# Optimization experiments

Hardware: AMD Instinct MI355X
Metric: run time of the kernel (lower is better)

The kernel has to match this reference:

```python
import jax, jax.numpy as jnp
import numpy as np

ALPHA = 0.01  # leaky relu slope

def setup_inputs() -> dict:
    key = jax.random.key(0)
    ks = jax.random.split(key, 6)
    B, N1, N2, D_IN, D_OUT = 8, 2048, 2048, 256, 256
    return {
        "input_tensor1": jax.random.normal(ks[0], (B, N1, D_IN), jnp.float32),
        "attention_mask1": jnp.zeros((B, 1, N1), jnp.float32),
        "input_tensor2": jax.random.normal(ks[1], (B, N2, D_IN), jnp.float32),
        "attention_mask2": jnp.zeros((B, 1, N2), jnp.float32),
        "W1": jax.random.normal(ks[2], (D_IN, D_OUT), jnp.float32) * 0.05,
        "a1": jax.random.normal(ks[3], (2 * D_OUT, 1), jnp.float32) * 0.05,
        "W2": jax.random.normal(ks[4], (D_IN, D_OUT), jnp.float32) * 0.05,
        "a2": jax.random.normal(ks[5], (2 * D_OUT, 1), jnp.float32) * 0.05,
    }

def _cross_attn(Wh_q, Wh_k, a, mask):
    d = Wh_q.shape[-1]
    # additive GAT-style scores: [B, Nq, 1] + [B, 1, Nk] -> [B, Nq, Nk]
    s_q = Wh_q @ a[:d, :]            # [B, Nq, 1]
    s_k = Wh_k @ a[d:, :]            # [B, Nk, 1]
    e = s_q + jnp.swapaxes(s_k, -1, -2)
    e = jax.nn.leaky_relu(e, negative_slope=ALPHA)
    probs = jax.nn.softmax(e + mask, axis=-1)
    ctx = probs @ Wh_k               # [B, Nq, d]
    return ctx, probs

def reference(input_tensor1, attention_mask1, input_tensor2, attention_mask2, W1, a1, W2, a2):
    # dropout in eval mode (identity) for a deterministic reference
    Wh11 = input_tensor1 @ W1
    Wh12 = input_tensor2 @ W1
    ctx1, probs1 = _cross_attn(Wh11, Wh12, a1, attention_mask2)
    Wh22 = input_tensor2 @ W2
    Wh21 = input_tensor1 @ W2
    ctx2, probs2 = _cross_attn(Wh22, Wh21, a2, attention_mask1)
    return ctx1, ctx2, probs1, probs2
```

## Files before the change

### kernel.cpp

```cpp
#include <hip/hip_runtime.h>
#include <hip/hip_bf16.h>
#include <stdint.h>

#define ALPHA 0.01f

typedef __attribute__((ext_vector_type(8))) short short8;
typedef __attribute__((ext_vector_type(4))) float f32x4;
typedef __attribute__((ext_vector_type(4))) float float4_;
typedef __attribute__((ext_vector_type(4))) unsigned short ushort4_;
typedef unsigned int u32;

static __device__ __forceinline__ unsigned short f2bf(float f) {
    union { float f; u32 u; } v; v.f = f;
    u32 r = v.u + 0x7FFF + ((v.u >> 16) & 1);
    return (unsigned short)(r >> 16);
}

static __device__ __forceinline__ void lds_load16(const void* g, void* l) {
    __builtin_amdgcn_global_load_lds((const __attribute__((address_space(1))) u32*)g,
                                     (__attribute__((address_space(3))) u32*)l, 16, 0, 0);
}

__global__ __launch_bounds__(256) void k_prep_w(const float* __restrict__ W1, const float* __restrict__ W2,
                                                unsigned short* __restrict__ W1T, unsigned short* __restrict__ W2T) {
    int bb = blockIdx.x;
    const float* W = (bb & 256) ? W2 : W1;
    unsigned short* WT = (bb & 256) ? W2T : W1T;
    int n = bb & 255, k = threadIdx.x;
    WT[n * 256 + k] = f2bf(W[k * 256 + n]);
}

__global__ __launch_bounds__(256) void k_prep_u(const float* __restrict__ W1, const float* __restrict__ a1,
                                                const float* __restrict__ W2, const float* __restrict__ a2,
                                                float* __restrict__ u) {
    int v = blockIdx.x;
    const float* W = (v < 2) ? W1 : W2;
    const float* a = ((v < 2) ? a1 : a2) + (v & 1) * 256;
    int d = threadIdx.x;
    float acc = 0.f;
    for (int n = 0; n < 256; n++) acc += W[d * 256 + n] * a[n];
    u[v * 256 + d] = acc;
}

__global__ __launch_bounds__(256) void k_cast_s(const float* __restrict__ in1, const float* __restrict__ in2,
                                                const float* __restrict__ u,
                                                unsigned short* __restrict__ in1b, unsigned short* __restrict__ in2b,
                                                float* __restrict__ s) {
    int gid = blockIdx.x * 4 + (threadIdx.x >> 6);
    int tensor = gid >> 14;
    int row = gid & 16383;
    int lane = threadIdx.x & 63;
    const float* in = tensor ? in2 : in1;
    unsigned short* outb = tensor ? in2b : in1b;
    const float* uA = u + (tensor ? 256 : 0);
    const float* uB = u + (tensor ? 512 : 768);
    float* sA = s + (tensor ? 1 : 0) * 16384;
    float* sB = s + (tensor ? 2 : 3) * 16384;

    float4_ v = *(const float4_*)(in + row * 256 + lane * 4);
    float4_ ua = *(const float4_*)(uA + lane * 4);
    float4_ ub = *(const float4_*)(uB + lane * 4);
    ushort4_ ob;
    ob.x = f2bf(v.x); ob.y = f2bf(v.y); ob.z = f2bf(v.z); ob.w = f2bf(v.w);
    *(ushort4_*)(outb + row * 256 + lane * 4) = ob;
    float accA = v.x * ua.x + v.y * ua.y + v.z * ua.z + v.w * ua.w;
    float accB = v.x * ub.x + v.y * ub.y + v.z * ub.z + v.w * ub.w;
    for (int off = 32; off; off >>= 1) {
        accA += __shfl_xor(accA, off, 64);
        accB += __shfl_xor(accB, off, 64);
    }
    if (lane == 0) { sA[row] = accA; sB[row] = accB; }
}

__global__ __launch_bounds__(256) void k_gemm_whT(const unsigned short* __restrict__ W1T,
                                                  const unsigned short* __restrict__ W2T,
                                                  const unsigned short* __restrict__ in1b,
                                                  const unsigned short* __restrict__ in2b,
                                                  unsigned short* __restrict__ whT1,
                                                  unsigned short* __restrict__ whT2) {
    __shared__ unsigned short sA[128 * 32];
    __shared__ unsigned short sB[128 * 32];
    int c = blockIdx.x >> 8;
    int bid = blockIdx.x & 255;
    int mt = bid & 1, ntile = bid >> 1;
    const unsigned short* A = c ? W2T : W1T;
    const unsigned short* Bm = c ? in1b : in2b;
    unsigned short* outp = c ? whT2 : whT1;
    int t = threadIdx.x;
    int w = t >> 6, lane = t & 63, l15 = lane & 15, lq = lane >> 4;
    int wm = (w & 1) * 64, wn = (w >> 1) * 64;
    f32x4 acc[4][4] = {};
    const unsigned short* gA = A + (mt * 128 + (t >> 2)) * 256 + (t & 3) * 8;
    const unsigned short* gB = Bm + (ntile * 128 + (t >> 2)) * 256 + (t & 3) * 8;

    for (int kk = 0; kk < 256; kk += 32) {
        lds_load16(gA + kk, &sA[t * 8]);
        lds_load16(gA + kk + 64 * 256, &sA[t * 8 + 2048]);
        lds_load16(gB + kk, &sB[t * 8]);
        lds_load16(gB + kk + 64 * 256, &sB[t * 8 + 2048]);
        __syncthreads();
        short8 af[4], bfr[4];
#pragma unroll
        for (int m2 = 0; m2 < 4; m2++) af[m2] = *(const short8*)&sA[(wm + m2 * 16 + l15) * 32 + lq * 8];
#pragma unroll
        for (int n2 = 0; n2 < 4; n2++) bfr[n2] = *(const short8*)&sB[(wn + n2 * 16 + l15) * 32 + lq * 8];
#pragma unroll
        for (int m2 = 0; m2 < 4; m2++)
#pragma unroll
            for (int n2 = 0; n2 < 4; n2++)
                acc[m2][n2] = __builtin_amdgcn_mfma_f32_16x16x32_bf16(af[m2], bfr[n2], acc[m2][n2], 0, 0, 0);
        __syncthreads();
    }
#pragma unroll
    for (int m2 = 0; m2 < 4; m2++) {
#pragma unroll
        for (int n2 = 0; n2 < 4; n2++) {
            int i_glob = ntile * 128 + wn + n2 * 16 + l15;
            int bb = i_glob >> 11, ii = i_glob & 2047;
#pragma unroll
            for (int r = 0; r < 4; r++) {
                int d = mt * 128 + wm + m2 * 16 + lq * 4 + r;
                outp[bb * (256 * 2048) + d * 2048 + ii] = f2bf(acc[m2][n2][r]);
            }
        }
    }
}

__global__ __launch_bounds__(512) void k_attn(const float* __restrict__ s,
                                              const unsigned short* __restrict__ whT1,
                                              const unsigned short* __restrict__ whT2,
                                              const float* __restrict__ mask1, const float* __restrict__ mask2,
                                              float* __restrict__ out) {
    __shared__ unsigned short sP[128 * 40];
    __shared__ unsigned short sV[256 * 32];
    __shared__ float lsk[2048];
    __shared__ float lmk[2048];
    __shared__ float lsq[128], lm[128], lil[128];

    int lb = (blockIdx.x & 7) * 32 + (blockIdx.x >> 3);
    int a = lb >> 7, b = (lb >> 4) & 7, mt = lb & 15;
    int t = threadIdx.x;
    const float* skp = s + (a ? 3 : 1) * 16384 + b * 2048;
    const float* sqp = s + (a ? 2 : 0) * 16384 + b * 2048 + mt * 128;
    const float* mp = (a ? mask1 : mask2) + b * 2048;
    const unsigned short* V = (a ? whT2 : whT1) + b * (256 * 2048);
    float* pout = out + 8388608 + a * 33554432 + (b * 2048 + mt * 128) * 2048;
    float* cout = out + a * 4194304 + (b * 2048 + mt * 128) * 256;

    for (int j = t; j < 2048; j += 512) { lsk[j] = skp[j]; lmk[j] = mp[j]; }
    if (t < 128) lsq[t] = sqp[t];
    __syncthreads();

    int w = t >> 6, lane = t & 63, l15 = lane & 15, lq = lane >> 4;

    for (int rr = 0; rr < 16; rr++) {
        int row = w * 16 + rr;
        float sq = lsq[row];
        float mx = -3.4e38f;
        for (int j = lane; j < 2048; j += 64) {
            float x = sq + lsk[j];
            x = fmaxf(x, x * ALPHA) + lmk[j];
            mx = fmaxf(mx, x);
        }
        for (int off = 32; off; off >>= 1) mx = fmaxf(mx, __shfl_xor(mx, off, 64));
        float sum = 0.f;
        for (int j = lane; j < 2048; j += 64) {
            float x = sq + lsk[j];
            x = fmaxf(x, x * ALPHA) + lmk[j];
            sum += __expf(x - mx);
        }
        for (int off = 32; off; off >>= 1) sum += __shfl_xor(sum, off, 64);
        if (lane == 0) { lm[row] = mx; lil[row] = 1.0f / sum; }
    }
    __syncthreads();

    int wm = (w & 1) * 64, wn = (w >> 1) * 64;
    f32x4 acc[4][4] = {};
    int pi = t >> 2;
    int pj = (t & 3) * 8;
    const unsigned short* gV = V + (t >> 2) * 2048 + (t & 3) * 8;

    for (int j0 = 0; j0 < 2048; j0 += 32) {
        lds_load16(gV + j0, &sV[t * 8]);
        lds_load16(gV + j0 + 128 * 2048, &sV[t * 8 + 4096]);
        __builtin_amdgcn_sched_barrier(0);

        float sqv = lsq[pi], mv = lm[pi], ilv = lil[pi];
        float pv[8];
#pragma unroll
        for (int q = 0; q < 8; q++) {
            float x = sqv + lsk[j0 + pj + q];
            x = fmaxf(x, x * ALPHA) + lmk[j0 + pj + q];
            pv[q] = __expf(x - mv) * ilv;
        }
        {
            float4_* gp = (float4_*)(pout + pi * 2048 + j0 + pj);
            float4_ v0, v1;
            v0.x = pv[0]; v0.y = pv[1]; v0.z = pv[2]; v0.w = pv[3];
            v1.x = pv[4]; v1.y = pv[5]; v1.z = pv[6]; v1.w = pv[7];
            __builtin_nontemporal_store(v0, gp);
            __builtin_nontemporal_store(v1, gp + 1);
        }
        union { short8 v; unsigned short u[8]; } pk;
#pragma unroll
        for (int q = 0; q < 8; q++) pk.u[q] = f2bf(pv[q]);
        *(short8*)&sP[pi * 40 + pj] = pk.v;

        asm volatile("s_waitcnt vmcnt(2) lgkmcnt(0)" ::: "memory");
        __builtin_amdgcn_s_barrier();

        short8 af[4], bfr[4];
#pragma unroll
        for (int m2 = 0; m2 < 4; m2++) af[m2] = *(const short8*)&sP[(wm + m2 * 16 + l15) * 40 + lq * 8];
#pragma unroll
        for (int n2 = 0; n2 < 4; n2++) bfr[n2] = *(const short8*)&sV[(wn + n2 * 16 + l15) * 32 + lq * 8];
#pragma unroll
        for (int m2 = 0; m2 < 4; m2++)
#pragma unroll
            for (int n2 = 0; n2 < 4; n2++)
                acc[m2][n2] = __builtin_amdgcn_mfma_f32_16x16x32_bf16(af[m2], bfr[n2], acc[m2][n2], 0, 0, 0);

        asm volatile("s_waitcnt lgkmcnt(0)" ::: "memory");
        __builtin_amdgcn_s_barrier();
    }

#pragma unroll
    for (int m2 = 0; m2 < 4; m2++) {
#pragma unroll
        for (int n2 = 0; n2 < 4; n2++) {
#pragma unroll
            for (int r = 0; r < 4; r++) {
                int i_loc = wm + m2 * 16 + lq * 4 + r;
                int d_loc = wn + n2 * 16 + l15;
                __builtin_nontemporal_store(acc[m2][n2][r], cout + i_loc * 256 + d_loc);
            }
        }
    }
}

extern "C" void kernel_launch(void* const* d_in, const int* in_sizes, int n_in,
                              void* d_out, int out_size, void* d_ws, size_t ws_size,
                              hipStream_t stream) {
    const float* in1   = (const float*)d_in[0];
    const float* mask1 = (const float*)d_in[1];
    const float* in2   = (const float*)d_in[2];
    const float* mask2 = (const float*)d_in[3];
    const float* W1    = (const float*)d_in[4];
    const float* a1    = (const float*)d_in[5];
    const float* W2    = (const float*)d_in[6];
    const float* a2    = (const float*)d_in[7];
    float* out = (float*)d_out;
    char* ws = (char*)d_ws;

    unsigned short* in1b = (unsigned short*)(ws);
    unsigned short* in2b = (unsigned short*)(ws + 8388608);
    unsigned short* whT1 = (unsigned short*)(ws + 16777216);
    unsigned short* whT2 = (unsigned short*)(ws + 25165824);
    unsigned short* W1T  = (unsigned short*)(ws + 33554432);
    unsigned short* W2T  = (unsigned short*)(ws + 33685504);
    float* u    = (float*)(ws + 33816576);
    float* s    = (float*)(ws + 33820672);

    k_prep_w<<<512, 256, 0, stream>>>(W1, W2, W1T, W2T);
    k_prep_u<<<4, 256, 0, stream>>>(W1, a1, W2, a2, u);
    k_cast_s<<<8192, 256, 0, stream>>>(in1, in2, u, in1b, in2b, s);
    k_gemm_whT<<<512, 256, 0, stream>>>(W1T, W2T, in1b, in2b, whT1, whT2);
    k_attn<<<256, 512, 0, stream>>>(s, whT1, whT2, mask1, mask2, out);
}
```

Baseline: 461.8 us.

## Double-buffer GEMM/attention LDS loads, use analytic row max, halve attention tile

Merges the two weight-prep kernels into one launch. Double-buffers the LDS tiles in the projection GEMM and in the attention PV loop so global-to-LDS loads for the next step overlap the MFMAs of the current one, and raises MFMA wave priority. In attention it replaces the per-row max pass with a bound computed from the global max of key scores and mask (valid because leaky-relu is monotone), uses exp2 with fma, and halves rows per block to 64 to launch 512 blocks. The bound-based max may underflow exponents if the mask has a wide spread, and the smaller tile does less V reuse per block.

```diff
diff --git a/kernel.cpp b/kernel.cpp
--- a/kernel.cpp
+++ b/kernel.cpp
@@ -21,25 +21,25 @@
                                      (__attribute__((address_space(3))) u32*)l, 16, 0, 0);
 }
 
-__global__ __launch_bounds__(256) void k_prep_w(const float* __restrict__ W1, const float* __restrict__ W2,
-                                                unsigned short* __restrict__ W1T, unsigned short* __restrict__ W2T) {
+__global__ __launch_bounds__(256) void k_prep(const float* __restrict__ W1, const float* __restrict__ a1,
+                                              const float* __restrict__ W2, const float* __restrict__ a2,
+                                              unsigned short* __restrict__ W1T, unsigned short* __restrict__ W2T,
+                                              float* __restrict__ u) {
     int bb = blockIdx.x;
-    const float* W = (bb & 256) ? W2 : W1;
-    unsigned short* WT = (bb & 256) ? W2T : W1T;
-    int n = bb & 255, k = threadIdx.x;
-    WT[n * 256 + k] = f2bf(W[k * 256 + n]);
-}
-
-__global__ __launch_bounds__(256) void k_prep_u(const float* __restrict__ W1, const float* __restrict__ a1,
-                                                const float* __restrict__ W2, const float* __restrict__ a2,
-                                                float* __restrict__ u) {
-    int v = blockIdx.x;
-    const float* W = (v < 2) ? W1 : W2;
-    const float* a = ((v < 2) ? a1 : a2) + (v & 1) * 256;
-    int d = threadIdx.x;
-    float acc = 0.f;
-    for (int n = 0; n < 256; n++) acc += W[d * 256 + n] * a[n];
-    u[v * 256 + d] = acc;
+    if (bb < 512) {
+        const float* W = (bb & 256) ? W2 : W1;
+        unsigned short* WT = (bb & 256) ? W2T : W1T;
+        int n = bb & 255, k = threadIdx.x;
+        WT[n * 256 + k] = f2bf(W[k * 256 + n]);
+    } else {
+        int v = bb - 512;
+        const float* W = (v < 2) ? W1 : W2;
+        const float* a = ((v < 2) ? a1 : a2) + (v & 1) * 256;
+        int d = threadIdx.x;
+        float acc = 0.f;
+        for (int n = 0; n < 256; n++) acc += W[d * 256 + n] * a[n];
+        u[v * 256 + d] = acc;
+    }
 }
 
 __global__ __launch_bounds__(256) void k_cast_s(const float* __restrict__ in1, const float* __restrict__ in2,
@@ -78,8 +78,8 @@
                                                   const unsigned short* __restrict__ in2b,
                                                   unsigned short* __restrict__ whT1,
                                                   unsigned short* __restrict__ whT2) {
-    __shared__ unsigned short sA[128 * 32];
-    __shared__ unsigned short sB[128 * 32];
+    __shared__ __attribute__((aligned(16))) unsigned short sA[2][128 * 32];
+    __shared__ __attribute__((aligned(16))) unsigned short sB[2][128 * 32];
     int c = blockIdx.x >> 8;
     int bid = blockIdx.x & 255;
     int mt = bid & 1, ntile = bid >> 1;
@@ -93,23 +93,39 @@
     const unsigned short* gA = A + (mt * 128 + (t >> 2)) * 256 + (t & 3) * 8;
     const unsigned short* gB = Bm + (ntile * 128 + (t >> 2)) * 256 + (t & 3) * 8;
 
-    for (int kk = 0; kk < 256; kk += 32) {
-        lds_load16(gA + kk, &sA[t * 8]);
-        lds_load16(gA + kk + 64 * 256, &sA[t * 8 + 2048]);
-        lds_load16(gB + kk, &sB[t * 8]);
-        lds_load16(gB + kk + 64 * 256, &sB[t * 8 + 2048]);
-        __syncthreads();
+    lds_load16(gA, &sA[0][t * 8]);
+    lds_load16(gA + 64 * 256, &sA[0][t * 8 + 2048]);
+    lds_load16(gB, &sB[0][t * 8]);
+    lds_load16(gB + 64 * 256, &sB[0][t * 8 + 2048]);
+
+    for (int it = 0; it < 8; ++it) {
+        int kn = ((it + 1) & 7) * 32;
+        unsigned short* dA = (unsigned short*)sA[(it + 1) & 1];
+        unsigned short* dB = (unsigned short*)sB[(it + 1) & 1];
+        lds_load16(gA + kn, dA + t * 8);
+        lds_load16(gA + kn + 64 * 256, dA + t * 8 + 2048);
+        lds_load16(gB + kn, dB + t * 8);
+        lds_load16(gB + kn + 64 * 256, dB + t * 8 + 2048);
+        __builtin_amdgcn_sched_barrier(0);
+        asm volatile("s_waitcnt vmcnt(4)" ::: "memory");
+        __builtin_amdgcn_s_barrier();
+
+        const unsigned short* cA = sA[it & 1];
+        const unsigned short* cB = sB[it & 1];
         short8 af[4], bfr[4];
 #pragma unroll
-        for (int m2 = 0; m2 < 4; m2++) af[m2] = *(const short8*)&sA[(wm + m2 * 16 + l15) * 32 + lq * 8];
-#pragma unroll
-        for (int n2 = 0; n2 < 4; n2++) bfr[n2] = *(const short8*)&sB[(wn + n2 * 16 + l15) * 32 + lq * 8];
+        for (int m2 = 0; m2 < 4; m2++) af[m2] = *(const short8*)&cA[(wm + m2 * 16 + l15) * 32 + lq * 8];
+#pragma unroll
+        for (int n2 = 0; n2 < 4; n2++) bfr[n2] = *(const short8*)&cB[(wn + n2 * 16 + l15) * 32 + lq * 8];
+        __builtin_amdgcn_s_setprio(1);
 #pragma unroll
         for (int m2 = 0; m2 < 4; m2++)
 #pragma unroll
             for (int n2 = 0; n2 < 4; n2++)
                 acc[m2][n2] = __builtin_amdgcn_mfma_f32_16x16x32_bf16(af[m2], bfr[n2], acc[m2][n2], 0, 0, 0);
-        __syncthreads();
+        __builtin_amdgcn_s_setprio(0);
+        asm volatile("s_waitcnt lgkmcnt(0)" ::: "memory");
+        __builtin_amdgcn_s_barrier();
     }
 #pragma unroll
     for (int m2 = 0; m2 < 4; m2++) {
@@ -126,112 +142,128 @@
     }
 }
 
-__global__ __launch_bounds__(512) void k_attn(const float* __restrict__ s,
-                                              const unsigned short* __restrict__ whT1,
-                                              const unsigned short* __restrict__ whT2,
-                                              const float* __restrict__ mask1, const float* __restrict__ mask2,
-                                              float* __restrict__ out) {
-    __shared__ unsigned short sP[128 * 40];
-    __shared__ unsigned short sV[256 * 32];
+__global__ __launch_bounds__(512, 4) void k_attn(const float* __restrict__ s,
+                                                 const unsigned short* __restrict__ whT1,
+                                                 const unsigned short* __restrict__ whT2,
+                                                 const float* __restrict__ mask1, const float* __restrict__ mask2,
+                                                 float* __restrict__ out) {
+    __shared__ __attribute__((aligned(16))) unsigned short sP[64 * 40];
+    __shared__ __attribute__((aligned(16))) unsigned short sV[2][256 * 32];
     __shared__ float lsk[2048];
     __shared__ float lmk[2048];
-    __shared__ float lsq[128], lm[128], lil[128];
-
-    int lb = (blockIdx.x & 7) * 32 + (blockIdx.x >> 3);
-    int a = lb >> 7, b = (lb >> 4) & 7, mt = lb & 15;
+    __shared__ float lsq[64], lmx[64], lil[64];
+    __shared__ float red[16];
+
+    int lb = (blockIdx.x & 7) * 64 + (blockIdx.x >> 3);
+    int a = lb >> 8, b = (lb >> 5) & 7, rg = lb & 31;
     int t = threadIdx.x;
     const float* skp = s + (a ? 3 : 1) * 16384 + b * 2048;
-    const float* sqp = s + (a ? 2 : 0) * 16384 + b * 2048 + mt * 128;
+    const float* sqp = s + (a ? 2 : 0) * 16384 + b * 2048 + rg * 64;
     const float* mp = (a ? mask1 : mask2) + b * 2048;
     const unsigned short* V = (a ? whT2 : whT1) + b * (256 * 2048);
-    float* pout = out + 8388608 + a * 33554432 + (b * 2048 + mt * 128) * 2048;
-    float* cout = out + a * 4194304 + (b * 2048 + mt * 128) * 256;
-
-    for (int j = t; j < 2048; j += 512) { lsk[j] = skp[j]; lmk[j] = mp[j]; }
-    if (t < 128) lsq[t] = sqp[t];
+    float* pout = out + 8388608 + a * 33554432 + (b * 2048 + rg * 64) * 2048;
+    float* cout = out + a * 4194304 + (b * 2048 + rg * 64) * 256;
+
+    float kmax = -3.4e38f, mmax = -3.4e38f;
+    for (int j = t; j < 2048; j += 512) {
+        float kv = skp[j], mv = mp[j];
+        lsk[j] = kv; lmk[j] = mv;
+        kmax = fmaxf(kmax, kv); mmax = fmaxf(mmax, mv);
+    }
+    if (t < 64) lsq[t] = sqp[t];
+    int w = t >> 6, lane = t & 63;
+    for (int off = 32; off; off >>= 1) {
+        kmax = fmaxf(kmax, __shfl_xor(kmax, off, 64));
+        mmax = fmaxf(mmax, __shfl_xor(mmax, off, 64));
+    }
+    if (lane == 0) { red[w] = kmax; red[8 + w] = mmax; }
     __syncthreads();
-
-    int w = t >> 6, lane = t & 63, l15 = lane & 15, lq = lane >> 4;
-
-    for (int rr = 0; rr < 16; rr++) {
-        int row = w * 16 + rr;
+    float skmax = fmaxf(fmaxf(fmaxf(red[0], red[1]), fmaxf(red[2], red[3])),
+                        fmaxf(fmaxf(red[4], red[5]), fmaxf(red[6], red[7])));
+    float mkmax = fmaxf(fmaxf(fmaxf(red[8], red[9]), fmaxf(red[10], red[11])),
+                        fmaxf(fmaxf(red[12], red[13]), fmaxf(red[14], red[15])));
+
+    const float L2E = 1.44269504f;
+    for (int rr = 0; rr < 8; rr++) {
+        int row = w * 8 + rr;
         float sq = lsq[row];
-        float mx = -3.4e38f;
-        for (int j = lane; j < 2048; j += 64) {
-            float x = sq + lsk[j];
-            x = fmaxf(x, x * ALPHA) + lmk[j];
-            mx = fmaxf(mx, x);
-        }
-        for (int off = 32; off; off >>= 1) mx = fmaxf(mx, __shfl_xor(mx, off, 64));
+        float mb = sq + skmax; mb = fmaxf(mb, mb * ALPHA) + mkmax;
+        float mL2 = mb * L2E;
         float sum = 0.f;
         for (int j = lane; j < 2048; j += 64) {
             float x = sq + lsk[j];
             x = fmaxf(x, x * ALPHA) + lmk[j];
-            sum += __expf(x - mx);
+            sum += exp2f(__builtin_fmaf(x, L2E, -mL2));
         }
         for (int off = 32; off; off >>= 1) sum += __shfl_xor(sum, off, 64);
-        if (lane == 0) { lm[row] = mx; lil[row] = 1.0f / sum; }
+        if (lane == 0) { lmx[row] = mL2; lil[row] = 1.0f / sum; }
     }
     __syncthreads();
 
-    int wm = (w & 1) * 64, wn = (w >> 1) * 64;
-    f32x4 acc[4][4] = {};
-    int pi = t >> 2;
-    int pj = (t & 3) * 8;
+    int l15 = lane & 15, lq = lane >> 4;
+    int wr = w >> 2, wc = w & 3;
+    f32x4 acc[2][4] = {};
+    int pi = t >> 3, pj = (t & 7) * 4;
     const unsigned short* gV = V + (t >> 2) * 2048 + (t & 3) * 8;
-
-    for (int j0 = 0; j0 < 2048; j0 += 32) {
-        lds_load16(gV + j0, &sV[t * 8]);
-        lds_load16(gV + j0 + 128 * 2048, &sV[t * 8 + 4096]);
+    float sqv = lsq[pi];
+    float mL2 = lmx[pi], ilv = lil[pi];
+    float* gp = pout + pi * 2048 + pj;
+    const float* lskp = lsk + pj;
+    const float* lmkp = lmk + pj;
+    unsigned short* sPp = sP + pi * 40 + pj;
+
+    lds_load16(gV, &sV[0][t * 8]);
+    lds_load16(gV + 128 * 2048, &sV[0][t * 8 + 4096]);
+
+    for (int it = 0; it < 64; ++it) {
+        int j0 = it * 32;
+        int jn = (j0 + 32) & 2047;
+        unsigned short* dst = (unsigned short*)sV[(it + 1) & 1];
+        lds_load16(gV + jn, dst + t * 8);
+        lds_load16(gV + jn + 128 * 2048, dst + t * 8 + 4096);
         __builtin_amdgcn_sched_barrier(0);
 
-        float sqv = lsq[pi], mv = lm[pi], ilv = lil[pi];
-        float pv[8];
-#pragma unroll
-        for (int q = 0; q < 8; q++) {
-            float x = sqv + lsk[j0 + pj + q];
-            x = fmaxf(x, x * ALPHA) + lmk[j0 + pj + q];
-            pv[q] = __expf(x - mv) * ilv;
+        float pv[4];
+#pragma unroll
+        for (int q = 0; q < 4; q++) {
+            float x = sqv + lskp[j0 + q];
+            x = fmaxf(x, x * ALPHA) + lmkp[j0 + q];
+            pv[q] = exp2f(__builtin_fmaf(x, L2E, -mL2)) * ilv;
         }
-        {
-            float4_* gp = (float4_*)(pout + pi * 2048 + j0 + pj);
-            float4_ v0, v1;
-            v0.x = pv[0]; v0.y = pv[1]; v0.z = pv[2]; v0.w = pv[3];
-            v1.x = pv[4]; v1.y = pv[5]; v1.z = pv[6]; v1.w = pv[7];
-            __builtin_nontemporal_store(v0, gp);
-            __builtin_nontemporal_store(v1, gp + 1);
-        }
-        union { short8 v; unsigned short u[8]; } pk;
-#pragma unroll
-        for (int q = 0; q < 8; q++) pk.u[q] = f2bf(pv[q]);
-        *(short8*)&sP[pi * 40 + pj] = pk.v;
-
-        asm volatile("s_waitcnt vmcnt(2) lgkmcnt(0)" ::: "memory");
+        float4_ v0; v0.x = pv[0]; v0.y = pv[1]; v0.z = pv[2]; v0.w = pv[3];
+        __builtin_nontemporal_store(v0, (float4_*)(gp + j0));
+        union { unsigned long long u64; unsigned short us[4]; } pk;
+        pk.us[0] = f2bf(pv[0]); pk.us[1] = f2bf(pv[1]); pk.us[2] = f2bf(pv[2]); pk.us[3] = f2bf(pv[3]);
+        *(unsigned long long*)sPp = pk.u64;
+
+        asm volatile("s_waitcnt vmcnt(3) lgkmcnt(0)" ::: "memory");
         __builtin_amdgcn_s_barrier();
 
-        short8 af[4], bfr[4];
-#pragma unroll
-        for (int m2 = 0; m2 < 4; m2++) af[m2] = *(const short8*)&sP[(wm + m2 * 16 + l15) * 40 + lq * 8];
-#pragma unroll
-        for (int n2 = 0; n2 < 4; n2++) bfr[n2] = *(const short8*)&sV[(wn + n2 * 16 + l15) * 32 + lq * 8];
-#pragma unroll
-        for (int m2 = 0; m2 < 4; m2++)
+        const unsigned short* sVc = sV[it & 1];
+        short8 af[2], bfr[4];
+#pragma unroll
+        for (int m2 = 0; m2 < 2; m2++) af[m2] = *(const short8*)&sP[(wr * 32 + m2 * 16 + l15) * 40 + lq * 8];
+#pragma unroll
+        for (int n2 = 0; n2 < 4; n2++) bfr[n2] = *(const short8*)&sVc[(wc * 64 + n2 * 16 + l15) * 32 + lq * 8];
+        __builtin_amdgcn_s_setprio(1);
+#pragma unroll
+        for (int m2 = 0; m2 < 2; m2++)
 #pragma unroll
             for (int n2 = 0; n2 < 4; n2++)
                 acc[m2][n2] = __builtin_amdgcn_mfma_f32_16x16x32_bf16(af[m2], bfr[n2], acc[m2][n2], 0, 0, 0);
-
+        __builtin_amdgcn_s_setprio(0);
         asm volatile("s_waitcnt lgkmcnt(0)" ::: "memory");
         __builtin_amdgcn_s_barrier();
     }
 
 #pragma unroll
-    for (int m2 = 0; m2 < 4; m2++) {
+    for (int m2 = 0; m2 < 2; m2++) {
 #pragma unroll
         for (int n2 = 0; n2 < 4; n2++) {
 #pragma unroll
             for (int r = 0; r < 4; r++) {
-                int i_loc = wm + m2 * 16 + lq * 4 + r;
-                int d_loc = wn + n2 * 16 + l15;
+                int i_loc = wr * 32 + m2 * 16 + lq * 4 + r;
+                int d_loc = wc * 64 + n2 * 16 + l15;
                 __builtin_nontemporal_store(acc[m2][n2][r], cout + i_loc * 256 + d_loc);
             }
         }
@@ -261,9 +293,8 @@
     float* u    = (float*)(ws + 33816576);
     float* s    = (float*)(ws + 33820672);
 
-    k_prep_w<<<512, 256, 0, stream>>>(W1, W2, W1T, W2T);
-    k_prep_u<<<4, 256, 0, stream>>>(W1, a1, W2, a2, u);
+    k_prep<<<516, 256, 0, stream>>>(W1, a1, W2, a2, W1T, W2T, u);
     k_cast_s<<<8192, 256, 0, stream>>>(in1, in2, u, in1b, in2b, s);
     k_gemm_whT<<<512, 256, 0, stream>>>(W1T, W2T, in1b, in2b, whT1, whT2);
-    k_attn<<<256, 512, 0, stream>>>(s, whT1, whT2, mask1, mask2, out);
-}
+    k_attn<<<512, 512, 0, stream>>>(s, whT1, whT2, mask1, mask2, out);
+}
```

Result: faster. 404.9 us (-12.3%).
